# Optimization experiments

Hardware: AMD Instinct MI355X
Metric: run time of the kernel (lower is better)

## Reference

```python
import jax, jax.numpy as jnp
import numpy as np

B, N, M, E = 2, 16384, 16384, 49152
W_CHAMFER, W_EDGE = 1.0, 0.1


def setup_inputs() -> dict:
    key = jax.random.key(0)
    k1, k2, k3 = jax.random.split(key, 3)
    pred_verts = jax.random.normal(k1, (B, N, 3), dtype=jnp.float32)
    target_verts = jax.random.normal(k2, (B, M, 3), dtype=jnp.float32)
    edges = jax.random.randint(k3, (E, 2), 0, N, dtype=jnp.int64)
    return {"pred_verts": pred_verts, "target_verts": target_verts, "edges": edges}


def reference(pred_verts, target_verts, edges):
    # --- Chamfer distance (torch.cdist + bidirectional min) ---
    # Squared-distance expansion avoids materializing the B x N x M x 3 diff tensor.
    p2 = jnp.sum(pred_verts * pred_verts, axis=-1)            # [B, N]
    t2 = jnp.sum(target_verts * target_verts, axis=-1)        # [B, M]
    cross = jnp.einsum('bnd,bmd->bnm', pred_verts, target_verts)  # [B, N, M]
    d2 = p2[:, :, None] + t2[:, None, :] - 2.0 * cross
    dist = jnp.sqrt(jnp.maximum(d2, 0.0))                     # [B, N, M]
    c_loss = jnp.mean(jnp.min(dist, axis=2)) + jnp.mean(jnp.min(dist, axis=1))

    # --- Edge-length variance regularization (vectorized over batch) ---
    v1 = pred_verts[:, edges[:, 0]]                           # [B, E, 3]
    v2 = pred_verts[:, edges[:, 1]]                           # [B, E, 3]
    edge_lengths = jnp.linalg.norm(v1 - v2, axis=-1)          # [B, E]
    # torch.var defaults to unbiased (ddof=1); mean over batch == sum/B
    e_loss = jnp.mean(jnp.var(edge_lengths, axis=1, ddof=1))

    total_loss = W_CHAMFER * c_loss + W_EDGE * e_loss
    return (total_loss, c_loss, e_loss)
```

## Files before the change

### kernel.cpp

```cpp
#include <hip/hip_runtime.h>
#include <float.h>

#define B_SZ 2
#define N_SZ 16384
#define E_SZ 49152

#define TPB 512
#define WAVES (TPB / 64)
#define ROWS_PER_BLOCK 256
#define CHUNK 1024
#define NCHUNK (N_SZ / CHUNK)
#define TILES_PER_CHUNK (CHUNK / 32)

#define CH_BLOCKS_PER_DIR (B_SZ * N_SZ / ROWS_PER_BLOCK)
#define CH_BLOCKS (2 * CH_BLOCKS_PER_DIR)
#define EDGE_BLOCKS (B_SZ * E_SZ / TPB)

#define PLANE_BYTES (N_SZ * 16)
#define BATCH_FRAG_BYTES (2 * PLANE_BYTES)
#define DIR_FRAG_BYTES (B_SZ * BATCH_FRAG_BYTES)
#define SUMS_OFF (2 * DIR_FRAG_BYTES)

typedef short short8 __attribute__((ext_vector_type(8)));
typedef float f32x16 __attribute__((ext_vector_type(16)));

__device__ inline short f2bf(float f) {
    unsigned u = __float_as_uint(f);
    unsigned r = (u + 0x7fffu + ((u >> 16) & 1u)) >> 16;
    return (short)r;
}
__device__ inline float bf2f(short s) {
    return __uint_as_float(((unsigned)(unsigned short)s) << 16);
}

__global__ __launch_bounds__(TPB) void prep(const float* __restrict__ pred,
                                            const float* __restrict__ tgt,
                                            char* __restrict__ ws) {
    int idx = blockIdx.x * TPB + threadIdx.x;
    double* sums = (double*)(ws + SUMS_OFF);
    if (blockIdx.x == 0 && threadIdx.x < 6) sums[threadIdx.x] = 0.0;

    const bool isTgt = idx < B_SZ * N_SZ;
    int row = isTgt ? idx : idx - B_SZ * N_SZ;
    int batch = row >> 14, pt = row & (N_SZ - 1);
    const float* src = (isTgt ? tgt : pred) + (size_t)row * 3;
    char* base = ws + (isTgt ? 0 : DIR_FRAG_BYTES) + (size_t)batch * BATCH_FRAG_BYTES;

    float tx = src[0], ty = src[1], tz = src[2];
    short hx = f2bf(tx), hy = f2bf(ty), hz = f2bf(tz);
    short lx = f2bf(tx - bf2f(hx)), ly = f2bf(ty - bf2f(hy)), lz = f2bf(tz - bf2f(hz));
    float t2 = fmaf(tx, tx, fmaf(ty, ty, tz * tz));
    short t2h = f2bf(t2), t2l = f2bf(t2 - bf2f(t2h));
    const short one = 0x3f80;

    *(short8*)(base + (size_t)pt * 16) = (short8){hx, hy, hz, hx, hy, hz, one, one};
    *(short8*)(base + PLANE_BYTES + (size_t)pt * 16) =
        (short8){lx, ly, lz, t2h, t2l, 0, 0, 0};
}

__global__ __launch_bounds__(TPB, 1) void main_kernel(
    const float* __restrict__ pred, const float* __restrict__ tgt,
    const int* __restrict__ edges, char* __restrict__ ws)
{
    __shared__ __align__(16) char sB[2][2 * CHUNK * 16];
    __shared__ float wred[WAVES], wred2[WAVES];
    double* sums = (double*)(ws + SUMS_OFF);
    const int lane = threadIdx.x & 63;
    const int wv = threadIdx.x >> 6;

    if (blockIdx.x < CH_BLOCKS) {
        const int dir = blockIdx.x >> 7;
        const int xb = blockIdx.x & 127;
        const int batch = xb >> 6;
        const int rowInB = (xb & 63) * ROWS_PER_BLOCK;
        const float* P = dir ? tgt : pred;
        const char* fragBase = ws + (size_t)dir * DIR_FRAG_BYTES
                                  + (size_t)batch * BATCH_FRAG_BYTES;
        const int bl = lane & 31;
        const int half = lane >> 5;

        int r = batch * N_SZ + rowInB + wv * 32 + bl;
        const float* p = P + (size_t)r * 3;
        float px = p[0], py = p[1], pz = p[2];
        float ax = -2.f * px, ay = -2.f * py, az = -2.f * pz;
        short ahx = f2bf(ax), ahy = f2bf(ay), ahz = f2bf(az);
        short alx = f2bf(ax - bf2f(ahx)), aly = f2bf(ay - bf2f(ahy)),
              alz = f2bf(az - bf2f(ahz));
        float p2 = fmaf(px, px, fmaf(py, py, pz * pz));
        short p2h = f2bf(p2), p2l = f2bf(p2 - bf2f(p2h));
        const short one = 0x3f80;
        short8 af = half == 0
            ? (short8){ahx, ahy, ahz, alx, aly, alz, p2h, p2l}
            : (short8){ahx, ahy, ahz, one, one, 0, 0, 0};

        const int t = threadIdx.x;
        float4 st0, st1, st2, st3;
        auto ldChunk = [&](int c) {
            const float4* s0 = (const float4*)(fragBase + (size_t)c * (CHUNK * 16));
            const float4* s1 = (const float4*)(fragBase + PLANE_BYTES + (size_t)c * (CHUNK * 16));
            st0 = s0[t]; st1 = s0[t + TPB]; st2 = s1[t]; st3 = s1[t + TPB];
        };
        auto wrChunk = [&](int buf) {
            float4* d = (float4*)sB[buf];
            d[t] = st0; d[t + TPB] = st1; d[t + 2 * TPB] = st2; d[t + 3 * TPB] = st3;
        };

        float nmin[16];
        #pragma unroll
        for (int e = 0; e < 16; e++) nmin[e] = FLT_MAX;
        const f32x16 zc = {0.f, 0.f, 0.f, 0.f, 0.f, 0.f, 0.f, 0.f,
                           0.f, 0.f, 0.f, 0.f, 0.f, 0.f, 0.f, 0.f};

        ldChunk(0); wrChunk(0);
        __syncthreads();

        for (int c = 0; c < NCHUNK; c++) {
            int buf = c & 1;
            if (c + 1 < NCHUNK) ldChunk(c + 1);
            const char* bp = sB[buf] + half * (CHUNK * 16) + bl * 16;
            #pragma unroll 2
            for (int mt = 0; mt < TILES_PER_CHUNK; mt += 2) {
                short8 b0 = *(const short8*)(bp + (mt * 32) * 16);
                short8 b1 = *(const short8*)(bp + (mt * 32 + 32) * 16);
                f32x16 r0 = __builtin_amdgcn_mfma_f32_32x32x16_bf16(af, b0, zc, 0, 0, 0);
                f32x16 r1 = __builtin_amdgcn_mfma_f32_32x32x16_bf16(af, b1, zc, 0, 0, 0);
                #pragma unroll
                for (int e = 0; e < 16; e++)
                    nmin[e] = fminf(fminf(r0[e], r1[e]), nmin[e]);
            }
            if (c + 1 < NCHUNK) wrChunk(buf ^ 1);
            __syncthreads();
        }

        float ssum = 0.f;
        #pragma unroll
        for (int e = 0; e < 16; e++) {
            float v = nmin[e];
            v = fminf(v, __shfl_xor(v, 1));
            v = fminf(v, __shfl_xor(v, 2));
            v = fminf(v, __shfl_xor(v, 4));
            v = fminf(v, __shfl_xor(v, 8));
            v = fminf(v, __shfl_xor(v, 16));
            ssum += sqrtf(fmaxf(v, 0.f));
        }
        ssum += __shfl_xor(ssum, 32);
        if (lane == 0) wred[wv] = ssum;
        __syncthreads();
        if (threadIdx.x == 0) {
            float total = 0.f;
            #pragma unroll
            for (int w = 0; w < WAVES; w++) total += wred[w];
            atomicAdd(&sums[dir], (double)total);
        }
    } else {
        int idx = (blockIdx.x - CH_BLOCKS) * TPB + threadIdx.x;
        int b = idx >= E_SZ;
        int e = idx - b * E_SZ;
        int2 ee = ((const int2*)edges)[e];
        const float* p0 = pred + ((size_t)b * N_SZ + (size_t)ee.x) * 3;
        const float* p1 = pred + ((size_t)b * N_SZ + (size_t)ee.y) * 3;
        float dx = p0[0] - p1[0], dy = p0[1] - p1[1], dz = p0[2] - p1[2];
        float len = sqrtf(dx * dx + dy * dy + dz * dz);
        float s = len, q = len * len;
        for (int o = 32; o > 0; o >>= 1) {
            s += __shfl_down(s, o, 64);
            q += __shfl_down(q, o, 64);
        }
        if (lane == 0) { wred[wv] = s; wred2[wv] = q; }
        __syncthreads();
        if (threadIdx.x == 0) {
            float ts = 0.f, tq = 0.f;
            #pragma unroll
            for (int w = 0; w < WAVES; w++) { ts += wred[w]; tq += wred2[w]; }
            atomicAdd(&sums[2 + 2 * b], (double)ts);
            atomicAdd(&sums[3 + 2 * b], (double)tq);
        }
    }
}

__global__ void final_kernel(const char* __restrict__ ws, float* __restrict__ out) {
    const double* sums = (const double*)(ws + SUMS_OFF);
    double c = sums[0] / (double)(B_SZ * N_SZ) + sums[1] / (double)(B_SZ * N_SZ);
    double e = 0.0;
    #pragma unroll
    for (int b = 0; b < B_SZ; b++) {
        double s = sums[2 + 2 * b], q = sums[3 + 2 * b];
        e += (q - s * s / (double)E_SZ) / (double)(E_SZ - 1);
    }
    e *= (1.0 / B_SZ);
    double tot = 1.0 * c + 0.1 * e;
    out[0] = (float)tot;
    out[1] = (float)c;
    out[2] = (float)e;
}

extern "C" void kernel_launch(void* const* d_in, const int* in_sizes, int n_in,
                              void* d_out, int out_size, void* d_ws, size_t ws_size,
                              hipStream_t stream) {
    const float* pred = (const float*)d_in[0];
    const float* tgt  = (const float*)d_in[1];
    const int* edges  = (const int*)d_in[2];
    float* out = (float*)d_out;
    char* ws = (char*)d_ws;

    prep<<<dim3((2 * B_SZ * N_SZ) / TPB), TPB, 0, stream>>>(pred, tgt, ws);

    main_kernel<<<dim3(CH_BLOCKS + EDGE_BLOCKS), TPB, 0, stream>>>(
        pred, tgt, edges, ws);

    final_kernel<<<dim3(1), dim3(1), 0, stream>>>(ws, out);
}
```

Baseline: 101.1 us.

## Split chamfer M-range across blocks with atomicMin row minima and parallel final reduce

Each chamfer block now scans only half of the opposite point set, doubling the chamfer block count to 512 so more CUs are busy. It also halves the chunk size and raises the occupancy hint to 4 blocks per CU. Per-row partial minima are merged in global memory with atomicMin on an order-preserving unsigned mapping of the floats. The final kernel becomes a 1024-thread reduction that applies sqrt and sums over all rows. The cost is extra atomics, a global minima buffer that prep must initialise, and a heavier final kernel.

```diff
diff --git a/kernel.cpp b/kernel.cpp
--- a/kernel.cpp
+++ b/kernel.cpp
@@ -8,18 +8,21 @@
 #define TPB 512
 #define WAVES (TPB / 64)
 #define ROWS_PER_BLOCK 256
-#define CHUNK 1024
-#define NCHUNK (N_SZ / CHUNK)
+#define MSPLIT 2
+#define MRANGE (N_SZ / MSPLIT)
+#define CHUNK 512
+#define NCHUNK (MRANGE / CHUNK)
 #define TILES_PER_CHUNK (CHUNK / 32)
 
-#define CH_BLOCKS_PER_DIR (B_SZ * N_SZ / ROWS_PER_BLOCK)
-#define CH_BLOCKS (2 * CH_BLOCKS_PER_DIR)
+#define CH_BLOCKS (2 * (B_SZ * N_SZ / ROWS_PER_BLOCK) * MSPLIT)
 #define EDGE_BLOCKS (B_SZ * E_SZ / TPB)
+#define NROWS_TOT (2 * B_SZ * N_SZ)
 
 #define PLANE_BYTES (N_SZ * 16)
 #define BATCH_FRAG_BYTES (2 * PLANE_BYTES)
 #define DIR_FRAG_BYTES (B_SZ * BATCH_FRAG_BYTES)
-#define SUMS_OFF (2 * DIR_FRAG_BYTES)
+#define MINS_OFF (2 * DIR_FRAG_BYTES)
+#define SUMS_OFF (MINS_OFF + NROWS_TOT * 4)
 
 typedef short short8 __attribute__((ext_vector_type(8)));
 typedef float f32x16 __attribute__((ext_vector_type(16)));
@@ -33,12 +36,23 @@
     return __uint_as_float(((unsigned)(unsigned short)s) << 16);
 }
 
+__device__ inline unsigned fmapu(float f) {
+    unsigned u = __float_as_uint(f);
+    return ((int)u < 0) ? ~u : (u ^ 0x80000000u);
+}
+__device__ inline float funmapu(unsigned v) {
+    unsigned b = ((int)v < 0) ? (v ^ 0x80000000u) : ~v;
+    return __uint_as_float(b);
+}
+
 __global__ __launch_bounds__(TPB) void prep(const float* __restrict__ pred,
                                             const float* __restrict__ tgt,
                                             char* __restrict__ ws) {
     int idx = blockIdx.x * TPB + threadIdx.x;
-    double* sums = (double*)(ws + SUMS_OFF);
-    if (blockIdx.x == 0 && threadIdx.x < 6) sums[threadIdx.x] = 0.0;
+    if (blockIdx.x == 0 && threadIdx.x < 6)
+        ((double*)(ws + SUMS_OFF))[threadIdx.x] = 0.0;
+    if (idx < NROWS_TOT) ((unsigned*)(ws + MINS_OFF))[idx] = 0xFFFFFFFFu;
+    if (idx >= 2 * B_SZ * N_SZ) return;
 
     const bool isTgt = idx < B_SZ * N_SZ;
     int row = isTgt ? idx : idx - B_SZ * N_SZ;
@@ -58,24 +72,28 @@
         (short8){lx, ly, lz, t2h, t2l, 0, 0, 0};
 }
 
-__global__ __launch_bounds__(TPB, 1) void main_kernel(
+__global__ __launch_bounds__(TPB, 4) void main_kernel(
     const float* __restrict__ pred, const float* __restrict__ tgt,
     const int* __restrict__ edges, char* __restrict__ ws)
 {
     __shared__ __align__(16) char sB[2][2 * CHUNK * 16];
     __shared__ float wred[WAVES], wred2[WAVES];
     double* sums = (double*)(ws + SUMS_OFF);
+    unsigned* minOut = (unsigned*)(ws + MINS_OFF);
     const int lane = threadIdx.x & 63;
     const int wv = threadIdx.x >> 6;
 
     if (blockIdx.x < CH_BLOCKS) {
-        const int dir = blockIdx.x >> 7;
-        const int xb = blockIdx.x & 127;
+        const int dir = blockIdx.x >> 8;
+        const int rest = blockIdx.x & 255;
+        const int ms = rest >> 7;
+        const int xb = rest & 127;
         const int batch = xb >> 6;
         const int rowInB = (xb & 63) * ROWS_PER_BLOCK;
         const float* P = dir ? tgt : pred;
         const char* fragBase = ws + (size_t)dir * DIR_FRAG_BYTES
                                   + (size_t)batch * BATCH_FRAG_BYTES;
+        const int mBase = ms * MRANGE;
         const int bl = lane & 31;
         const int half = lane >> 5;
 
@@ -94,15 +112,16 @@
             : (short8){ahx, ahy, ahz, one, one, 0, 0, 0};
 
         const int t = threadIdx.x;
-        float4 st0, st1, st2, st3;
+        float4 st0, st1;
         auto ldChunk = [&](int c) {
-            const float4* s0 = (const float4*)(fragBase + (size_t)c * (CHUNK * 16));
-            const float4* s1 = (const float4*)(fragBase + PLANE_BYTES + (size_t)c * (CHUNK * 16));
-            st0 = s0[t]; st1 = s0[t + TPB]; st2 = s1[t]; st3 = s1[t + TPB];
+            const float4* s0 = (const float4*)(fragBase + (size_t)(mBase + c * CHUNK) * 16);
+            const float4* s1 = (const float4*)(fragBase + PLANE_BYTES
+                                               + (size_t)(mBase + c * CHUNK) * 16);
+            st0 = s0[t]; st1 = s1[t];
         };
         auto wrChunk = [&](int buf) {
             float4* d = (float4*)sB[buf];
-            d[t] = st0; d[t + TPB] = st1; d[t + 2 * TPB] = st2; d[t + 3 * TPB] = st3;
+            d[t] = st0; d[t + TPB] = st1;
         };
 
         float nmin[16];
@@ -118,21 +137,27 @@
             int buf = c & 1;
             if (c + 1 < NCHUNK) ldChunk(c + 1);
             const char* bp = sB[buf] + half * (CHUNK * 16) + bl * 16;
-            #pragma unroll 2
-            for (int mt = 0; mt < TILES_PER_CHUNK; mt += 2) {
-                short8 b0 = *(const short8*)(bp + (mt * 32) * 16);
-                short8 b1 = *(const short8*)(bp + (mt * 32 + 32) * 16);
+            for (int g = 0; g < TILES_PER_CHUNK / 4; g++) {
+                short8 b0 = *(const short8*)(bp + (g * 128 + 0) * 16);
+                short8 b1 = *(const short8*)(bp + (g * 128 + 32) * 16);
+                short8 b2 = *(const short8*)(bp + (g * 128 + 64) * 16);
+                short8 b3 = *(const short8*)(bp + (g * 128 + 96) * 16);
                 f32x16 r0 = __builtin_amdgcn_mfma_f32_32x32x16_bf16(af, b0, zc, 0, 0, 0);
                 f32x16 r1 = __builtin_amdgcn_mfma_f32_32x32x16_bf16(af, b1, zc, 0, 0, 0);
+                f32x16 r2 = __builtin_amdgcn_mfma_f32_32x32x16_bf16(af, b2, zc, 0, 0, 0);
+                f32x16 r3 = __builtin_amdgcn_mfma_f32_32x32x16_bf16(af, b3, zc, 0, 0, 0);
                 #pragma unroll
-                for (int e = 0; e < 16; e++)
-                    nmin[e] = fminf(fminf(r0[e], r1[e]), nmin[e]);
+                for (int e = 0; e < 16; e++) {
+                    float u = fminf(r0[e], r1[e]);
+                    float v = fminf(r2[e], r3[e]);
+                    nmin[e] = fminf(fminf(u, v), nmin[e]);
+                }
             }
             if (c + 1 < NCHUNK) wrChunk(buf ^ 1);
             __syncthreads();
         }
 
-        float ssum = 0.f;
+        float vals[16];
         #pragma unroll
         for (int e = 0; e < 16; e++) {
             float v = nmin[e];
@@ -141,16 +166,15 @@
             v = fminf(v, __shfl_xor(v, 4));
             v = fminf(v, __shfl_xor(v, 8));
             v = fminf(v, __shfl_xor(v, 16));
-            ssum += sqrtf(fmaxf(v, 0.f));
-        }
-        ssum += __shfl_xor(ssum, 32);
-        if (lane == 0) wred[wv] = ssum;
-        __syncthreads();
-        if (threadIdx.x == 0) {
-            float total = 0.f;
+            vals[e] = v;
+        }
+        if (bl == 0) {
+            int base = dir * (B_SZ * N_SZ) + batch * N_SZ + rowInB + wv * 32 + half * 4;
             #pragma unroll
-            for (int w = 0; w < WAVES; w++) total += wred[w];
-            atomicAdd(&sums[dir], (double)total);
+            for (int e = 0; e < 16; e++) {
+                int rrow = (e & 3) + 8 * (e >> 2);
+                atomicMin(&minOut[base + rrow], fmapu(vals[e]));
+            }
         }
     } else {
         int idx = (blockIdx.x - CH_BLOCKS) * TPB + threadIdx.x;
@@ -178,20 +202,45 @@
     }
 }
 
-__global__ void final_kernel(const char* __restrict__ ws, float* __restrict__ out) {
+#define FIN_TPB 1024
+__global__ __launch_bounds__(FIN_TPB) void final_kernel(const char* __restrict__ ws,
+                                                        float* __restrict__ out) {
+    const uint4* mins = (const uint4*)(ws + MINS_OFF);
     const double* sums = (const double*)(ws + SUMS_OFF);
-    double c = sums[0] / (double)(B_SZ * N_SZ) + sums[1] / (double)(B_SZ * N_SZ);
-    double e = 0.0;
+    __shared__ double redA[FIN_TPB / 64], redB[FIN_TPB / 64];
+
+    float sA = 0.f, sB = 0.f;
     #pragma unroll
-    for (int b = 0; b < B_SZ; b++) {
-        double s = sums[2 + 2 * b], q = sums[3 + 2 * b];
-        e += (q - s * s / (double)E_SZ) / (double)(E_SZ - 1);
-    }
-    e *= (1.0 / B_SZ);
-    double tot = 1.0 * c + 0.1 * e;
-    out[0] = (float)tot;
-    out[1] = (float)c;
-    out[2] = (float)e;
+    for (int i = 0; i < 16; i++) {
+        uint4 v = mins[i * FIN_TPB + threadIdx.x];
+        float s = sqrtf(fmaxf(funmapu(v.x), 0.f)) + sqrtf(fmaxf(funmapu(v.y), 0.f))
+                + sqrtf(fmaxf(funmapu(v.z), 0.f)) + sqrtf(fmaxf(funmapu(v.w), 0.f));
+        if (i < 8) sA += s; else sB += s;
+    }
+    for (int o = 32; o > 0; o >>= 1) {
+        sA += __shfl_down(sA, o, 64);
+        sB += __shfl_down(sB, o, 64);
+    }
+    int wv = threadIdx.x >> 6, ln = threadIdx.x & 63;
+    if (ln == 0) { redA[wv] = (double)sA; redB[wv] = (double)sB; }
+    __syncthreads();
+    if (threadIdx.x == 0) {
+        double tA = 0.0, tB = 0.0;
+        #pragma unroll
+        for (int w = 0; w < FIN_TPB / 64; w++) { tA += redA[w]; tB += redB[w]; }
+        double c = tA / (double)(B_SZ * N_SZ) + tB / (double)(B_SZ * N_SZ);
+        double e = 0.0;
+        #pragma unroll
+        for (int b = 0; b < B_SZ; b++) {
+            double s = sums[2 + 2 * b], q = sums[3 + 2 * b];
+            e += (q - s * s / (double)E_SZ) / (double)(E_SZ - 1);
+        }
+        e *= (1.0 / B_SZ);
+        double tot = 1.0 * c + 0.1 * e;
+        out[0] = (float)tot;
+        out[1] = (float)c;
+        out[2] = (float)e;
+    }
 }
 
 extern "C" void kernel_launch(void* const* d_in, const int* in_sizes, int n_in,
@@ -208,5 +257,5 @@
     main_kernel<<<dim3(CH_BLOCKS + EDGE_BLOCKS), TPB, 0, stream>>>(
         pred, tgt, edges, ws);
 
-    final_kernel<<<dim3(1), dim3(1), 0, stream>>>(ws, out);
-}
+    final_kernel<<<dim3(1), FIN_TPB, 0, stream>>>(ws, out);
+}
```

After: 174.5 us. 1.73x slower.
